# Optimization experiments

Measured on AMD Instinct MI355X. Metric: run time of the kernel, lower is better.

The kernel has to match this reference:

```python
import jax, jax.numpy as jnp
import numpy as np

BATCH, SEQ, DIN, FILTERS, KSIZE = 64, 512, 256, 256, 3

def setup_inputs() -> dict:
    key = jax.random.key(0)
    ks = jax.random.split(key, 5)
    s_u = 1.0 / np.sqrt(DIN)
    return {
        "x": jax.random.normal(ks[0], (BATCH, SEQ, DIN), dtype=jnp.float32),
        "z": jax.random.normal(ks[1], (BATCH, DIN), dtype=jnp.float32),
        "U": jax.random.normal(ks[2], (DIN, DIN), dtype=jnp.float32) * s_u,
        "V": jax.random.normal(ks[3], (DIN, KSIZE * FILTERS), dtype=jnp.float32) * s_u,
        "B_w": jax.random.normal(ks[4], (DIN, KSIZE * FILTERS), dtype=jnp.float32) * s_u,
        "b": jnp.zeros((FILTERS,), dtype=jnp.float32),
        "kernel_size": KSIZE,
    }

def reference(x, z, U, V, B_w, b, kernel_size):
    Bn, L, din = x.shape
    K = int(kernel_size)
    F = V.shape[1] // K
    # per-sample dynamic kernel: (U * sigmoid(z)) @ V + B
    zf = jax.nn.sigmoid(z)                                  # (B, din)
    f = jnp.einsum('de,be,ef->bdf', U, zf, V) + B_w[None]    # (B, din, K*F)
    f = f.reshape(Bn, din, K, F).transpose(0, 2, 1, 3)       # (B, K, din, F)
    # 'same' padding, stride 1
    pad_l, pad_r = (K - 1) // 2, K // 2
    xp = jnp.pad(x, ((0, 0), (pad_l, pad_r), (0, 0)))        # (B, L+K-1, din)
    patches = jnp.stack([xp[:, i:i + L] for i in range(K)], axis=2)  # (B, L, K, din)
    out = jnp.einsum('blkd,bkdf->blf', patches, f) + b       # (B, L, F)
    return jax.nn.relu(out)
```

## Files before the change

kernel.cpp:

```cpp
#include <hip/hip_runtime.h>
#include <math.h>

#define BATCH 64
#define SEQL  512
#define DIN   256
#define NF    256
#define KS    3
#define KF    (KS * NF)

#define XCH 512
#define KC  (KS * XCH)
#define PR2 66
#define PLD 128
#define P0SZ (PR2 * PLD)

typedef __attribute__((ext_vector_type(8))) short short8;
typedef __attribute__((ext_vector_type(4))) float floatx4;
typedef __attribute__((ext_vector_type(16))) float floatx16;
typedef __attribute__((ext_vector_type(8))) unsigned short ushort8v;
typedef __attribute__((ext_vector_type(4))) unsigned short ushort4v;

static __device__ __forceinline__ unsigned short f2bf(float f) {
    unsigned int u = __float_as_uint(f);
    return (unsigned short)((u + 0x7FFF + ((u >> 16) & 1)) >> 16);
}

__global__ __launch_bounds__(256) void pack_kernel(
    const float* __restrict__ U, const float* __restrict__ V,
    const float* __restrict__ Bw,
    unsigned short* __restrict__ WcTp, unsigned short* __restrict__ UTp)
{
    const int blk = blockIdx.x;
    const int t   = threadIdx.x;

    if (blk < 96) {
        const int gk = blk >> 3;
        const int g  = gk / 3, k = gk % 3;
        const int ks = t >> 5;
        const int f  = (blk & 7) * 32 + (t & 31);
        unsigned short* dst = WcTp + ((size_t)(gk * 8 + ks) * 256 + f) * 16;
        #pragma unroll
        for (int c = 0; c < 16; ++c) {
            const int ch = g * 128 + ks * 16 + c;
            const float v = (ch < DIN)
                ? Bw[(size_t)ch * KF + k * NF + f]
                : V[(size_t)(ch - DIN) * KF + k * NF + f];
            dst[c] = f2bf(v);
        }
    } else {
        const int bb = blk - 96;
        const int kk = bb >> 1;
        const int e0 = (bb & 1) * 128;
        #pragma unroll
        for (int it = 0; it < 2; ++it) {
            const int p    = t + it * 256;
            const int e    = e0 + (p >> 2);
            const int quad = p & 3;
            unsigned short* dst =
                UTp + ((size_t)(kk * 256 + e) * 4 + quad) * 8;
            #pragma unroll
            for (int c = 0; c < 8; ++c) {
                const int d = kk * 32 + quad * 8 + c;
                dst[c] = f2bf(U[(size_t)d * DIN + e]);
            }
        }
    }
}

__global__ __launch_bounds__(256, 2) void fused_kernel(
    const float* __restrict__ x, const float* __restrict__ z,
    const unsigned short* __restrict__ UTp,
    const unsigned short* __restrict__ WcTp,
    const float* __restrict__ bias, float* __restrict__ out)
{
    __shared__ __align__(16) unsigned short lds[4 * P0SZ];

    const int tid  = threadIdx.x;
    const int lane = tid & 63;
    const int wave = tid >> 6;
    const int quad = lane >> 4, l16 = lane & 15;
    const int l32  = lane & 31, hi  = lane >> 5;

    const int bid = blockIdx.x;
    const int b   = bid >> 3;
    const int l0  = (bid & 7) * 64;

    short8 uA[4], uB[4];
    auto loadU = [&](int kk, short8 (&buf)[4]) {
        #pragma unroll
        for (int q = 0; q < 4; ++q) {
            const int e = q * 64 + wave * 16 + l16;
            buf[q] = *(const short8*)
                &UTp[((size_t)(kk * 256 + e) * 4 + quad) * 8];
        }
    };

    loadU(0, uA);

    #pragma unroll
    for (int p = 0; p < 2; ++p) {
        unsigned short* P = lds + (size_t)p * P0SZ;
        #pragma unroll
        for (int it = 0; it < 5; ++it) {
            const int idx = tid + it * 256;
            if (idx < PR2 * 16) {
                const int row = idx >> 4, u = idx & 15;
                const int l = l0 - 1 + row;
                ushort8v h = {};
                if (l >= 0 && l < SEQL) {
                    const float* xp =
                        x + ((size_t)b * SEQL + l) * DIN + p * 128 + u * 8;
                    const float4 v0 = *(const float4*)xp;
                    const float4 v1 = *(const float4*)(xp + 4);
                    h[0] = f2bf(v0.x); h[1] = f2bf(v0.y);
                    h[2] = f2bf(v0.z); h[3] = f2bf(v0.w);
                    h[4] = f2bf(v1.x); h[5] = f2bf(v1.y);
                    h[6] = f2bf(v1.z); h[7] = f2bf(v1.w);
                }
                *(ushort8v*)&P[row * PLD + ((u ^ (row & 15)) << 3)] = h;
            }
        }
    }
    __syncthreads();

    floatx4 accY[4][5] = {};
    {
        auto computeG = [&](int kk, const short8 (&buf)[4]) {
            const unsigned short* P = lds + (size_t)(kk >> 2) * P0SZ;
            const int ux = (kk & 3) * 4 + quad;
            __builtin_amdgcn_s_setprio(1);
            #pragma unroll
            for (int i = 0; i < 5; ++i) {
                const int row = i * 16 + l16;
                const short8 xf = *(const short8*)
                    &P[row * PLD + ((ux ^ (row & 15)) << 3)];
                #pragma unroll
                for (int q = 0; q < 4; ++q)
                    accY[q][i] = __builtin_amdgcn_mfma_f32_16x16x32_bf16(
                        buf[q], xf, accY[q][i], 0, 0, 0);
            }
            __builtin_amdgcn_s_setprio(0);
        };
        #pragma unroll 1
        for (int kb = 0; kb < 4; ++kb) {
            const int kk = kb * 2;
            loadU(kk + 1, uB);
            computeG(kk, uA);
            if (kk + 2 < 8) loadU(kk + 2, uA);
            computeG(kk + 1, uB);
        }
    }

    short8 bA[16], bB[16];
    auto loadB = [&](int r, short8 (&buf)[16]) {
        const int gg = r / 3, k = r - gg * 3;
        const int g  = (gg + (bid & 3)) & 3;
        const unsigned short* gW = WcTp + (size_t)(g * 3 + k) * 8 * 4096;
        #pragma unroll
        for (int ks = 0; ks < 8; ++ks)
            #pragma unroll
            for (int j = 0; j < 2; ++j) {
                const int f = wave * 64 + j * 32 + l32;
                buf[ks * 2 + j] = *(const short8*)
                    &gW[(size_t)ks * 4096 + (size_t)f * 16 + hi * 8];
            }
    };

    loadB(0, bA);

    #pragma unroll
    for (int q = 0; q < 4; ++q) {
        const int e0 = q * 64 + wave * 16 + quad * 4;
        unsigned short* PY = lds + (size_t)(2 + (q >> 1)) * P0SZ;
        const int c0 = e0 & 127;
        float zf[4];
        #pragma unroll
        for (int r2 = 0; r2 < 4; ++r2)
            zf[r2] = 1.0f / (1.0f + expf(-z[(size_t)b * DIN + e0 + r2]));
        const int u = c0 >> 3;
        #pragma unroll
        for (int i = 0; i < 5; ++i) {
            const int xrow = i * 16 + l16;
            if (xrow < PR2) {
                ushort4v h;
                #pragma unroll
                for (int r2 = 0; r2 < 4; ++r2)
                    h[r2] = f2bf(accY[q][i][r2] * zf[r2]);
                *(ushort4v*)&PY[xrow * PLD + ((u ^ (xrow & 15)) << 3) +
                                (c0 & 7)] = h;
            }
        }
    }
    __syncthreads();

    floatx16 acc2[2][2] = {};
    {
        auto computeB = [&](int r, const short8 (&buf)[16]) {
            const int gg = r / 3, k = r - gg * 3;
            const int g  = (gg + (bid & 3)) & 3;
            const unsigned short* P = lds + (size_t)g * P0SZ;
            __builtin_amdgcn_s_setprio(1);
            #pragma unroll
            for (int ks = 0; ks < 8; ++ks) {
                short8 af[2];
                const int ua = ks * 2 + hi;
                #pragma unroll
                for (int i = 0; i < 2; ++i) {
                    const int m = i * 32 + l32 + k;
                    af[i] = *(const short8*)
                        &P[m * PLD + ((ua ^ (m & 15)) << 3)];
                }
                #pragma unroll
                for (int i = 0; i < 2; ++i)
                    #pragma unroll
                    for (int j = 0; j < 2; ++j)
                        acc2[i][j] = __builtin_amdgcn_mfma_f32_32x32x16_bf16(
                            af[i], buf[ks * 2 + j], acc2[i][j], 0, 0, 0);
            }
            __builtin_amdgcn_s_setprio(0);
        };
        #pragma unroll 1
        for (int rr = 0; rr < 6; ++rr) {
            const int r = rr * 2;
            loadB(r + 1, bB);
            computeB(r, bA);
            if (r + 2 < 12) loadB(r + 2, bA);
            computeB(r + 1, bB);
        }
    }

    #pragma unroll
    for (int j = 0; j < 2; ++j) {
        const int f  = wave * 64 + j * 32 + l32;
        const float bv = bias[f];
        #pragma unroll
        for (int i = 0; i < 2; ++i) {
            #pragma unroll
            for (int reg = 0; reg < 16; ++reg) {
                const int rowl = i * 32 + (reg & 3) + 8 * (reg >> 2) + 4 * hi;
                const float v = acc2[i][j][reg] + bv;
                out[((size_t)b * SEQL + l0 + rowl) * NF + f] = fmaxf(v, 0.0f);
            }
        }
    }
}

extern "C" void kernel_launch(void* const* d_in, const int* in_sizes, int n_in,
                              void* d_out, int out_size, void* d_ws, size_t ws_size,
                              hipStream_t stream) {
    const float* x    = (const float*)d_in[0];
    const float* z    = (const float*)d_in[1];
    const float* U    = (const float*)d_in[2];
    const float* V    = (const float*)d_in[3];
    const float* Bw   = (const float*)d_in[4];
    const float* bias = (const float*)d_in[5];

    unsigned short* WcTp = (unsigned short*)d_ws;
    unsigned short* UTp  = WcTp + (size_t)12 * 8 * 256 * 16;
    float* out = (float*)d_out;

    pack_kernel<<<dim3(112), 256, 0, stream>>>(U, V, Bw, WcTp, UTp);
    fused_kernel<<<dim3(512), 256, 0, stream>>>(x, z, UTp, WcTp, bias, out);
}
```

Baseline: 121.7 us.

## Split fused kernel work across eight waves per block instead of four

Doubles the block size to 512 threads and divides each wave's share of the work in half. In the first GEMM each wave now covers two e-slices instead of four, and in the second each wave covers one 32-wide filter slice instead of two, with the weight-fragment prefetch split into half-k chunks. The aim is fewer registers per wave and more waves in flight to hide memory and LDS latency. In exchange, each weight fragment is reused across fewer MFMAs, LDS A-fragment reads are duplicated across more waves, and there are more pipeline iterations.

Result: slower. 126.2 us (+3.7%).

```diff
diff --git a/kernel.cpp b/kernel.cpp
--- a/kernel.cpp
+++ b/kernel.cpp
@@ -67,7 +67,7 @@
     }
 }
 
-__global__ __launch_bounds__(256, 2) void fused_kernel(
+__global__ __launch_bounds__(512, 4) void fused_kernel(
     const float* __restrict__ x, const float* __restrict__ z,
     const unsigned short* __restrict__ UTp,
     const unsigned short* __restrict__ WcTp,
@@ -85,11 +85,11 @@
     const int b   = bid >> 3;
     const int l0  = (bid & 7) * 64;
 
-    short8 uA[4], uB[4];
-    auto loadU = [&](int kk, short8 (&buf)[4]) {
-        #pragma unroll
-        for (int q = 0; q < 4; ++q) {
-            const int e = q * 64 + wave * 16 + l16;
+    short8 uA[2], uB[2];
+    auto loadU = [&](int kk, short8 (&buf)[2]) {
+        #pragma unroll
+        for (int q = 0; q < 2; ++q) {
+            const int e = q * 128 + wave * 16 + l16;
             buf[q] = *(const short8*)
                 &UTp[((size_t)(kk * 256 + e) * 4 + quad) * 8];
         }
@@ -101,8 +101,8 @@
     for (int p = 0; p < 2; ++p) {
         unsigned short* P = lds + (size_t)p * P0SZ;
         #pragma unroll
-        for (int it = 0; it < 5; ++it) {
-            const int idx = tid + it * 256;
+        for (int it = 0; it < 3; ++it) {
+            const int idx = tid + it * 512;
             if (idx < PR2 * 16) {
                 const int row = idx >> 4, u = idx & 15;
                 const int l = l0 - 1 + row;
@@ -123,9 +123,9 @@
     }
     __syncthreads();
 
-    floatx4 accY[4][5] = {};
+    floatx4 accY[2][5] = {};
     {
-        auto computeG = [&](int kk, const short8 (&buf)[4]) {
+        auto computeG = [&](int kk, const short8 (&buf)[2]) {
             const unsigned short* P = lds + (size_t)(kk >> 2) * P0SZ;
             const int ux = (kk & 3) * 4 + quad;
             __builtin_amdgcn_s_setprio(1);
@@ -135,7 +135,7 @@
                 const short8 xf = *(const short8*)
                     &P[row * PLD + ((ux ^ (row & 15)) << 3)];
                 #pragma unroll
-                for (int q = 0; q < 4; ++q)
+                for (int q = 0; q < 2; ++q)
                     accY[q][i] = __builtin_amdgcn_mfma_f32_16x16x32_bf16(
                         buf[q], xf, accY[q][i], 0, 0, 0);
             }
@@ -151,27 +151,26 @@
         }
     }
 
-    short8 bA[16], bB[16];
-    auto loadB = [&](int r, short8 (&buf)[16]) {
+    short8 cA[4], cB[4];
+    auto loadH = [&](int h, short8 (&buf)[4]) {
+        const int r  = h >> 1;
         const int gg = r / 3, k = r - gg * 3;
         const int g  = (gg + (bid & 3)) & 3;
         const unsigned short* gW = WcTp + (size_t)(g * 3 + k) * 8 * 4096;
-        #pragma unroll
-        for (int ks = 0; ks < 8; ++ks)
-            #pragma unroll
-            for (int j = 0; j < 2; ++j) {
-                const int f = wave * 64 + j * 32 + l32;
-                buf[ks * 2 + j] = *(const short8*)
-                    &gW[(size_t)ks * 4096 + (size_t)f * 16 + hi * 8];
-            }
+        const int ks0 = (h & 1) * 4;
+        const int f   = wave * 32 + l32;
+        #pragma unroll
+        for (int ks2 = 0; ks2 < 4; ++ks2)
+            buf[ks2] = *(const short8*)
+                &gW[(size_t)(ks0 + ks2) * 4096 + (size_t)f * 16 + hi * 8];
     };
 
-    loadB(0, bA);
+    loadH(0, cA);
 
     #pragma unroll
-    for (int q = 0; q < 4; ++q) {
-        const int e0 = q * 64 + wave * 16 + quad * 4;
-        unsigned short* PY = lds + (size_t)(2 + (q >> 1)) * P0SZ;
+    for (int q = 0; q < 2; ++q) {
+        const int e0 = q * 128 + wave * 16 + quad * 4;
+        unsigned short* PY = lds + (size_t)(2 + q) * P0SZ;
         const int c0 = e0 & 127;
         float zf[4];
         #pragma unroll
@@ -193,15 +192,18 @@
     }
     __syncthreads();
 
-    floatx16 acc2[2][2] = {};
+    floatx16 acc2[2] = {};
     {
-        auto computeB = [&](int r, const short8 (&buf)[16]) {
+        auto computeH = [&](int h, const short8 (&buf)[4]) {
+            const int r  = h >> 1;
             const int gg = r / 3, k = r - gg * 3;
             const int g  = (gg + (bid & 3)) & 3;
             const unsigned short* P = lds + (size_t)g * P0SZ;
+            const int ks0 = (h & 1) * 4;
             __builtin_amdgcn_s_setprio(1);
             #pragma unroll
-            for (int ks = 0; ks < 8; ++ks) {
+            for (int ks2 = 0; ks2 < 4; ++ks2) {
+                const int ks = ks0 + ks2;
                 short8 af[2];
                 const int ua = ks * 2 + hi;
                 #pragma unroll
@@ -212,33 +214,30 @@
                 }
                 #pragma unroll
                 for (int i = 0; i < 2; ++i)
-                    #pragma unroll
-                    for (int j = 0; j < 2; ++j)
-                        acc2[i][j] = __builtin_amdgcn_mfma_f32_32x32x16_bf16(
-                            af[i], buf[ks * 2 + j], acc2[i][j], 0, 0, 0);
+                    acc2[i] = __builtin_amdgcn_mfma_f32_32x32x16_bf16(
+                        af[i], buf[ks2], acc2[i], 0, 0, 0);
             }
             __builtin_amdgcn_s_setprio(0);
         };
         #pragma unroll 1
-        for (int rr = 0; rr < 6; ++rr) {
-            const int r = rr * 2;
-            loadB(r + 1, bB);
-            computeB(r, bA);
-            if (r + 2 < 12) loadB(r + 2, bA);
-            computeB(r + 1, bB);
-        }
-    }
-
-    #pragma unroll
-    for (int j = 0; j < 2; ++j) {
-        const int f  = wave * 64 + j * 32 + l32;
+        for (int hh = 0; hh < 12; ++hh) {
+            const int h = hh * 2;
+            loadH(h + 1, cB);
+            computeH(h, cA);
+            if (h + 2 < 24) loadH(h + 2, cA);
+            computeH(h + 1, cB);
+        }
+    }
+
+    {
+        const int f  = wave * 32 + l32;
         const float bv = bias[f];
         #pragma unroll
         for (int i = 0; i < 2; ++i) {
             #pragma unroll
             for (int reg = 0; reg < 16; ++reg) {
                 const int rowl = i * 32 + (reg & 3) + 8 * (reg >> 2) + 4 * hi;
-                const float v = acc2[i][j][reg] + bv;
+                const float v = acc2[i][reg] + bv;
                 out[((size_t)b * SEQL + l0 + rowl) * NF + f] = fmaxf(v, 0.0f);
             }
         }
@@ -260,5 +259,5 @@
     float* out = (float*)d_out;
 
     pack_kernel<<<dim3(112), 256, 0, stream>>>(U, V, Bw, WcTp, UTp);
-    fused_kernel<<<dim3(512), 256, 0, stream>>>(x, z, UTp, WcTp, bias, out);
-}
+    fused_kernel<<<dim3(512), 512, 0, stream>>>(x, z, UTp, WcTp, bias, out);
+}
```
